# Kernel tuning notes

Measured on AMD Instinct MI355X. Metric: run time of the kernel, lower is better.

The kernel has to match this reference:

```python
import jax, jax.numpy as jnp
import numpy as np

EPS = 1e-06


def setup_inputs() -> dict:
    key = jax.random.key(0)
    ks = jax.random.split(key, 8)
    B, T, D = 4, 1024, 1024  # module requires T == D (diagonal einsum)
    s = 1.0 / np.sqrt(D)
    return {
        "x_seq": jax.random.normal(ks[0], (B, T, D), dtype=jnp.float32),
        "gamma": jnp.asarray(0.9, dtype=jnp.float32),
        "Wq": jax.random.normal(ks[1], (D, D), dtype=jnp.float32) * s,
        "bq": jax.random.normal(ks[2], (D,), dtype=jnp.float32) * 0.01,
        "Wk": jax.random.normal(ks[3], (D, D), dtype=jnp.float32) * s,
        "bk": jax.random.normal(ks[4], (D,), dtype=jnp.float32) * 0.01,
        "Wv": jax.random.normal(ks[5], (D, D), dtype=jnp.float32) * s,
        "bv": jax.random.normal(ks[6], (D,), dtype=jnp.float32) * 0.01,
    }


def reference(x_seq, gamma, Wq, bq, Wk, bk, Wv, bv):
    # Faithful math of SUPRAParallelFixedGamma.forward. Notes on fidelity:
    # - torch einsum 'ij,bjdj->bidj' takes the DIAGONAL of kv over (time, last
    #   v-dim), i.e. kv[b,j,d,j] = k[b,j,d] * v[b,j,j]; requires T == D.
    # - gamma_exponents = arange(T)[None,:] - arange(T)[:,None] -> E[i,j] = max(j-i, 0)
    #   (the clamp leaves PAST entries at gamma**0 == 1 and decays FUTURE ones).
    # - S = cumsum over dim 1 (the 'i'/time-output axis) then contracted with q;
    #   this factors exactly as C = cumsum(G, axis=0) applied as a (T,T) weight,
    #   avoiding the original's O(B*T*D*T) intermediate while computing the same math.
    B, T, D = x_seq.shape
    q = jax.nn.relu(x_seq @ Wq.T + bq)          # phi(W_q x)
    k = jax.nn.relu(x_seq @ Wk.T + bk)          # phi(W_k x)
    v = x_seq @ Wv.T + bv
    t = jnp.arange(T)
    E = jnp.maximum(t[None, :] - t[:, None], 0).astype(x_seq.dtype)  # (T,T)
    G = gamma ** E                               # gamma_powers[i,j] = gamma**max(j-i,0)
    C = jnp.cumsum(G, axis=0)                    # C[t,j] = sum_{t'<=t} G[t',j]
    vd = jnp.diagonal(v, axis1=1, axis2=2)       # (B,T): v[b,j,j]  (T==D)
    kv_diag = k * vd[:, :, None]                 # (B,T,D): kv[b,j,d,j]
    # num[b,t,j] = sum_d q[b,t,d] * C[t,j] * kv_diag[b,j,d]
    num = C[None, :, :] * jnp.einsum('btd,bjd->btj', q, kv_diag)
    # Z[b,t,d] = cumsum_t of (G @ k) = sum_j C[t,j] k[b,j,d]
    Z = jnp.einsum('tj,bjd->btd', C, k)
    denom = jnp.sum(q * Z, axis=-1, keepdims=True) + EPS
    return num / denom
```

## Files before the change

kernel.cpp:

```cpp
#include <hip/hip_runtime.h>

typedef __attribute__((ext_vector_type(8))) short bf16x8;
typedef __attribute__((ext_vector_type(4))) float f32x4;


__device__ __forceinline__ unsigned short f2bf(float f) {
    unsigned int u = __builtin_bit_cast(unsigned int, f);
    u += 0x7fffu + ((u >> 16) & 1u);
    return (unsigned short)(u >> 16);
}

__device__ __forceinline__ float bf2f(unsigned short s) {
    return __builtin_bit_cast(float, (unsigned int)s << 16);
}

__device__ __forceinline__ void g2lds16(const unsigned short* g, unsigned short* l) {
    __builtin_amdgcn_global_load_lds(
        (const __attribute__((address_space(1))) unsigned int*)g,
        (__attribute__((address_space(3))) unsigned int*)l, 16, 0, 0);
}


__global__ __launch_bounds__(256)
void prep_kernel(const float* __restrict__ x, const float* __restrict__ wq,
                 const float* __restrict__ wk, const float* __restrict__ Wv,
                 const float* __restrict__ bv, unsigned short* __restrict__ xb,
                 unsigned short* __restrict__ wqk, float* __restrict__ vd,
                 int n4x, int n4w, int npack) {
    if ((int)blockIdx.x < npack) {
        int i = blockIdx.x * 256 + threadIdx.x;
        const float* src; unsigned short* dst; int idx;
        if (i < n4x)            { src = x;  dst = xb;  idx = i; }
        else if (i < n4x + n4w) { src = wq; dst = wqk; idx = i - n4x; }
        else                    { src = wk; dst = wqk + (size_t)n4w * 4; idx = i - n4x - n4w; }
        float4 v = reinterpret_cast<const float4*>(src)[idx];
        union { unsigned short s[4]; uint2 u; } o;
        o.s[0] = f2bf(v.x); o.s[1] = f2bf(v.y); o.s[2] = f2bf(v.z); o.s[3] = f2bf(v.w);
        reinterpret_cast<uint2*>(dst)[idx] = o.u;
    } else {
        int w = (blockIdx.x - npack) * 4 + (threadIdx.x >> 6);
        int lane = threadIdx.x & 63;
        int b = w >> 10, j = w & 1023;
        const float4* xr = reinterpret_cast<const float4*>(x + (size_t)(b * 1024 + j) * 1024);
        const float4* wr = reinterpret_cast<const float4*>(Wv + (size_t)j * 1024);
        float s = 0.f;
        #pragma unroll
        for (int e = 0; e < 4; ++e) {
            float4 a = xr[lane + 64 * e], c = wr[lane + 64 * e];
            s += a.x * c.x + a.y * c.y + a.z * c.z + a.w * c.w;
        }
        #pragma unroll
        for (int off = 32; off; off >>= 1) s += __shfl_down(s, off, 64);
        if (lane == 0) vd[w] = s + bv[j];
    }
}


__global__ __launch_bounds__(256, 2)
void gemm_qk_kernel(const unsigned short* __restrict__ A, const unsigned short* __restrict__ Bm,
                    unsigned short* __restrict__ qb, unsigned short* __restrict__ kb,
                    const float* __restrict__ bq, const float* __restrict__ bk, int K) {
    __shared__ unsigned short lA[2][128 * 32];
    __shared__ unsigned short lB[2][128 * 32];

    const int tid = threadIdx.x;
    const int lane = tid & 63;
    const int wid = tid >> 6;
    const int wr = wid >> 1;
    const int wc = wid & 1;
    const int tileM = blockIdx.y * 128, tileN = blockIdx.x * 128;

    const int srow = tid >> 2;
    const int scolL = (tid & 3) * 8;
    const int scolG = ((tid & 3) ^ (srow & 3)) * 8;
    const int frow = lane & 15;
    const int fq = lane >> 4;
    const int gR = (fq ^ (frow & 3)) * 8;

    f32x4 acc[4][4];
    #pragma unroll
    for (int m = 0; m < 4; ++m)
        #pragma unroll
        for (int n = 0; n < 4; ++n)
            acc[m][n] = (f32x4){0.f, 0.f, 0.f, 0.f};

    auto stage = [&](int buf, int k0) {
        g2lds16(A + (size_t)(tileM + srow) * K + (k0 + scolG),      &lA[buf][srow * 32 + scolL]);
        g2lds16(A + (size_t)(tileM + 64 + srow) * K + (k0 + scolG), &lA[buf][(64 + srow) * 32 + scolL]);
        g2lds16(Bm + (size_t)(tileN + srow) * K + (k0 + scolG),     &lB[buf][srow * 32 + scolL]);
        g2lds16(Bm + (size_t)(tileN + 64 + srow) * K + (k0 + scolG),&lB[buf][(64 + srow) * 32 + scolL]);
    };

    stage(0, 0);
    __syncthreads();
    int cur = 0;
    for (int k0 = 0; k0 < K; k0 += 32) {
        if (k0 + 32 < K) stage(cur ^ 1, k0 + 32);

        bf16x8 af[4], bfr[4];
        #pragma unroll
        for (int m = 0; m < 4; ++m)
            af[m] = *reinterpret_cast<const bf16x8*>(
                &lA[cur][(wr * 64 + m * 16 + frow) * 32 + gR]);
        #pragma unroll
        for (int n = 0; n < 4; ++n)
            bfr[n] = *reinterpret_cast<const bf16x8*>(
                &lB[cur][(wc * 64 + n * 16 + frow) * 32 + gR]);

        #pragma unroll
        for (int m = 0; m < 4; ++m)
            #pragma unroll
            for (int n = 0; n < 4; ++n)
                acc[m][n] = __builtin_amdgcn_mfma_f32_16x16x32_bf16(af[m], bfr[n], acc[m][n], 0, 0, 0);

        __syncthreads();
        cur ^= 1;
    }

    const int orow = (lane >> 4) * 4;
    const int ocol = lane & 15;
    const bool isQ = tileN < 1024;
    unsigned short* Cq = isQ ? qb : kb;
    const float* bias = isQ ? bq : bk;
    const int cb = tileN - (isQ ? 0 : 1024);

    #pragma unroll
    for (int n = 0; n < 4; ++n) {
        int col = cb + wc * 64 + n * 16 + ocol;
        float bia = bias[col];
        #pragma unroll
        for (int m = 0; m < 4; ++m) {
            #pragma unroll
            for (int i = 0; i < 4; ++i) {
                int row = tileM + wr * 64 + m * 16 + orow + i;
                float v = acc[m][n][i] + bia;
                Cq[(size_t)row * 1024 + col] = f2bf(v > 0.f ? v : 0.f);
            }
        }
    }
}


__global__ __launch_bounds__(256, 3)
void gemm_attn_kernel(const unsigned short* __restrict__ A, const unsigned short* __restrict__ Bm,
                      unsigned short* __restrict__ nmb, const float* __restrict__ vd,
                      float* __restrict__ dpart, const float* __restrict__ gammap,
                      int K, int Mtot) {
    __shared__ unsigned short lA[2][64 * 32];
    __shared__ unsigned short lB[2][128 * 32];

    const int tid = threadIdx.x;
    const int lane = tid & 63;
    const int wid = tid >> 6;
    const int wr = wid >> 1, wc = wid & 1;
    const int tileM = blockIdx.y * 64, tileN = blockIdx.x * 128;

    const unsigned short* Ab = A + (size_t)blockIdx.z * 1024 * 1024;
    const unsigned short* Bb = Bm + (size_t)blockIdx.z * 1024 * 1024;

    const int r0 = tid >> 2;
    const int r1 = (tid + 256) >> 2;
    const int cc = (tid & 3) * 8;
    const int frow = lane & 15;
    const int fk = (lane >> 4) * 8;

    f32x4 acc[2][4];
    #pragma unroll
    for (int m = 0; m < 2; ++m)
        #pragma unroll
        for (int n = 0; n < 4; ++n)
            acc[m][n] = (f32x4){0.f, 0.f, 0.f, 0.f};

    auto stage = [&](int buf, int k0) {
        g2lds16(Ab + (size_t)(tileM + r0) * K + (k0 + cc), &lA[buf][tid * 8]);
        g2lds16(Bb + (size_t)(tileN + r0) * K + (k0 + cc), &lB[buf][tid * 8]);
        g2lds16(Bb + (size_t)(tileN + r1) * K + (k0 + cc), &lB[buf][2048 + tid * 8]);
    };

    stage(0, 0);
    __syncthreads();
    int cur = 0;
    for (int k0 = 0; k0 < K; k0 += 32) {
        if (k0 + 32 < K) stage(cur ^ 1, k0 + 32);

        bf16x8 af[2], bfr[4];
        #pragma unroll
        for (int m = 0; m < 2; ++m)
            af[m] = *reinterpret_cast<const bf16x8*>(&lA[cur][(wr * 32 + m * 16 + frow) * 32 + fk]);
        #pragma unroll
        for (int n = 0; n < 4; ++n)
            bfr[n] = *reinterpret_cast<const bf16x8*>(&lB[cur][(wc * 64 + n * 16 + frow) * 32 + fk]);

        #pragma unroll
        for (int m = 0; m < 2; ++m)
            #pragma unroll
            for (int n = 0; n < 4; ++n)
                acc[m][n] = __builtin_amdgcn_mfma_f32_16x16x32_bf16(af[m], bfr[n], acc[m][n], 0, 0, 0);

        __syncthreads();
        cur ^= 1;
    }

    const int orow = (lane >> 4) * 4;
    const int ocol = lane & 15;

    unsigned short* ob = nmb + (size_t)blockIdx.z * 1024 * 1024;
    const float* vdb = vd + blockIdx.z * 1024;
    const float g = gammap[0];
    const float l2g = log2f(g);
    const float inv1mg = 1.f / (1.f - g);
    const float c1 = g * inv1mg;

    int jcol[4]; float gj[4], vdv[4];
    #pragma unroll
    for (int n = 0; n < 4; ++n) {
        jcol[n] = tileN + wc * 64 + n * 16 + ocol;
        gj[n] = exp2f((float)jcol[n] * l2g);
        vdv[n] = vdb[jcol[n]];
    }

    #pragma unroll
    for (int m = 0; m < 2; ++m) {
        #pragma unroll
        for (int i = 0; i < 4; ++i) {
            int t = tileM + wr * 32 + m * 16 + orow + i;
            float gt = exp2f((float)t * l2g);
            float ctf = (1.f - g * gt) * inv1mg;
            float s = 0.f;
            #pragma unroll
            for (int n = 0; n < 4; ++n) {
                int j = jcol[n];
                float Cfut = exp2f((float)(j - t) * l2g) * ctf;
                float Cpast = (float)(t - j + 1) + c1 * (1.f - gj[n]);
                float Cw = (j <= t) ? Cpast : Cfut;
                float v = acc[m][n][i];
                s += Cw * v;
                ob[(size_t)t * 1024 + j] = f2bf(Cw * vdv[n] * v);
            }
            s += __shfl_xor(s, 1, 64);
            s += __shfl_xor(s, 2, 64);
            s += __shfl_xor(s, 4, 64);
            s += __shfl_xor(s, 8, 64);
            if ((lane & 15) == 0)
                dpart[(size_t)(blockIdx.x * 2 + wc) * Mtot + blockIdx.z * 1024 + t] = s;
        }
    }
}


__global__ __launch_bounds__(256)
void scale_kernel(const unsigned short* __restrict__ nmb, float* __restrict__ out,
                  const float* __restrict__ dpart, int Mtot) {
    int r = blockIdx.x;
    float s = 1e-6f;
    #pragma unroll
    for (int p = 0; p < 16; ++p) s += dpart[(size_t)p * Mtot + r];
    float inv = 1.f / s;
    const uint2* src = reinterpret_cast<const uint2*>(nmb + (size_t)r * 1024);
    float4* dst = reinterpret_cast<float4*>(out + (size_t)r * 1024);
    uint2 u = src[threadIdx.x];
    float4 v = { bf2f((unsigned short)(u.x & 0xffff)) * inv,
                 bf2f((unsigned short)(u.x >> 16))    * inv,
                 bf2f((unsigned short)(u.y & 0xffff)) * inv,
                 bf2f((unsigned short)(u.y >> 16))    * inv };
    dst[threadIdx.x] = v;
}


extern "C" void kernel_launch(void* const* d_in, const int* in_sizes, int n_in,
                              void* d_out, int out_size, void* d_ws, size_t ws_size,
                              hipStream_t stream) {
    const float* x     = (const float*)d_in[0];
    const float* gamma = (const float*)d_in[1];
    const float* Wq    = (const float*)d_in[2];
    const float* bq    = (const float*)d_in[3];
    const float* Wk    = (const float*)d_in[4];
    const float* bk    = (const float*)d_in[5];
    const float* Wv    = (const float*)d_in[6];
    const float* bv    = (const float*)d_in[7];
    float* out = (float*)d_out;

    const int D = 1024, T = 1024;
    const int B = in_sizes[0] / (T * D);
    const int M = B * T;

    char* ws = (char*)d_ws;
    size_t off = 0;
    unsigned short* xb  = (unsigned short*)(ws + off); off += (size_t)M * D * 2;
    unsigned short* wqk = (unsigned short*)(ws + off); off += (size_t)2 * D * D * 2;
    unsigned short* qb  = (unsigned short*)(ws + off); off += (size_t)M * D * 2;
    unsigned short* kb  = (unsigned short*)(ws + off); off += (size_t)M * D * 2;
    float* vd    = (float*)(ws + off); off += (size_t)M * 4;
    float* dpart = (float*)(ws + off); off += (size_t)16 * M * 4;
    unsigned short* nmb = xb;

    const int n4x = M * D / 4, n4w = D * D / 4;
    const int npack = (n4x + 2 * n4w) / 256;

    prep_kernel<<<dim3(npack + M / 4), 256, 0, stream>>>(
        x, Wq, Wk, Wv, bv, xb, wqk, vd, n4x, n4w, npack);

    gemm_qk_kernel<<<dim3(2048 / 128, M / 128), 256, 0, stream>>>(
        xb, wqk, qb, kb, bq, bk, D);

    gemm_attn_kernel<<<dim3(T / 128, T / 64, B), 256, 0, stream>>>(
        qb, kb, nmb, vd, dpart, gamma, D, M);

    scale_kernel<<<dim3(M), 256, 0, stream>>>(nmb, out, dpart, M);
}
```

Measured before the change: 75.13 us.

## Enlarge QK GEMM tiles to 256x256 with 4-slot async LDS pipeline

The Q/K projection GEMM moves from 128x128 tiles with 256 threads and double buffering to 256x256 tiles with 512 threads, a 4-slot LDS ring that prefetches two stages ahead, and explicit vmcnt waits with a single barrier per k-step. The MFMA loop is raised in priority via s_setprio, and A fragments are loaded per m-row to limit register pressure. The aim is more reuse per LDS load and better overlap of global-to-LDS copies with MFMA. The trade-offs are that the XOR swizzle is dropped, which may cause LDS bank conflicts, LDS use grows to 128 KB, and the grid shrinks to 128 blocks, which may underfill the GPU.

```diff
diff --git a/kernel.cpp b/kernel.cpp
--- a/kernel.cpp
+++ b/kernel.cpp
@@ -56,65 +56,71 @@
 }
 
 
-__global__ __launch_bounds__(256, 2)
+__global__ __launch_bounds__(512, 2)
 void gemm_qk_kernel(const unsigned short* __restrict__ A, const unsigned short* __restrict__ Bm,
                     unsigned short* __restrict__ qb, unsigned short* __restrict__ kb,
                     const float* __restrict__ bq, const float* __restrict__ bk, int K) {
-    __shared__ unsigned short lA[2][128 * 32];
-    __shared__ unsigned short lB[2][128 * 32];
+    __shared__ unsigned short lA[4][256 * 32];
+    __shared__ unsigned short lB[4][256 * 32];
 
     const int tid = threadIdx.x;
     const int lane = tid & 63;
     const int wid = tid >> 6;
-    const int wr = wid >> 1;
-    const int wc = wid & 1;
-    const int tileM = blockIdx.y * 128, tileN = blockIdx.x * 128;
-
-    const int srow = tid >> 2;
-    const int scolL = (tid & 3) * 8;
-    const int scolG = ((tid & 3) ^ (srow & 3)) * 8;
+    const int wm = wid >> 2;
+    const int wn = wid & 3;
+    const int tileM = blockIdx.y * 256, tileN = blockIdx.x * 256;
+
     const int frow = lane & 15;
-    const int fq = lane >> 4;
-    const int gR = (fq ^ (frow & 3)) * 8;
-
-    f32x4 acc[4][4];
-    #pragma unroll
-    for (int m = 0; m < 4; ++m)
+    const int fq8 = (lane >> 4) * 8;
+
+    const int sr0 = wid * 16 + (lane >> 2);
+    const int sc = (lane & 3) * 8;
+
+    f32x4 acc[8][4];
+    #pragma unroll
+    for (int m = 0; m < 8; ++m)
         #pragma unroll
         for (int n = 0; n < 4; ++n)
             acc[m][n] = (f32x4){0.f, 0.f, 0.f, 0.f};
 
-    auto stage = [&](int buf, int k0) {
-        g2lds16(A + (size_t)(tileM + srow) * K + (k0 + scolG),      &lA[buf][srow * 32 + scolL]);
-        g2lds16(A + (size_t)(tileM + 64 + srow) * K + (k0 + scolG), &lA[buf][(64 + srow) * 32 + scolL]);
-        g2lds16(Bm + (size_t)(tileN + srow) * K + (k0 + scolG),     &lB[buf][srow * 32 + scolL]);
-        g2lds16(Bm + (size_t)(tileN + 64 + srow) * K + (k0 + scolG),&lB[buf][(64 + srow) * 32 + scolL]);
+    auto stage = [&](int slot, int k0) {
+        #pragma unroll
+        for (int j = 0; j < 2; ++j) {
+            int r = sr0 + j * 128;
+            g2lds16(A + (size_t)(tileM + r) * K + (k0 + sc), &lA[slot][r * 32 + sc]);
+            g2lds16(Bm + (size_t)(tileN + r) * K + (k0 + sc), &lB[slot][r * 32 + sc]);
+        }
     };
 
+    const int nS = K >> 5;
     stage(0, 0);
-    __syncthreads();
-    int cur = 0;
-    for (int k0 = 0; k0 < K; k0 += 32) {
-        if (k0 + 32 < K) stage(cur ^ 1, k0 + 32);
-
-        bf16x8 af[4], bfr[4];
-        #pragma unroll
-        for (int m = 0; m < 4; ++m)
-            af[m] = *reinterpret_cast<const bf16x8*>(
-                &lA[cur][(wr * 64 + m * 16 + frow) * 32 + gR]);
+    stage(1, 32);
+
+    for (int s = 0; s < nS; ++s) {
+        const int slot = s & 3;
+        if (s + 1 < nS) asm volatile("s_waitcnt vmcnt(4)" ::: "memory");
+        else            asm volatile("s_waitcnt vmcnt(0)" ::: "memory");
+        __builtin_amdgcn_s_barrier();
+        asm volatile("" ::: "memory");
+
+        if (s + 2 < nS) stage((s + 2) & 3, (s + 2) << 5);
+
+        bf16x8 bfr[4];
         #pragma unroll
         for (int n = 0; n < 4; ++n)
             bfr[n] = *reinterpret_cast<const bf16x8*>(
-                &lB[cur][(wc * 64 + n * 16 + frow) * 32 + gR]);
-
-        #pragma unroll
-        for (int m = 0; m < 4; ++m)
+                &lB[slot][(wn * 64 + n * 16 + frow) * 32 + fq8]);
+
+        __builtin_amdgcn_s_setprio(1);
+        #pragma unroll
+        for (int m = 0; m < 8; ++m) {
+            bf16x8 af = *reinterpret_cast<const bf16x8*>(
+                &lA[slot][(wm * 128 + m * 16 + frow) * 32 + fq8]);
             #pragma unroll
             for (int n = 0; n < 4; ++n)
-                acc[m][n] = __builtin_amdgcn_mfma_f32_16x16x32_bf16(af[m], bfr[n], acc[m][n], 0, 0, 0);
-
-        __syncthreads();
-        cur ^= 1;
+                acc[m][n] = __builtin_amdgcn_mfma_f32_16x16x32_bf16(af, bfr[n], acc[m][n], 0, 0, 0);
+        }
+        __builtin_amdgcn_s_setprio(0);
     }
 
     const int orow = (lane >> 4) * 4;
@@ -126,13 +132,13 @@
 
     #pragma unroll
     for (int n = 0; n < 4; ++n) {
-        int col = cb + wc * 64 + n * 16 + ocol;
+        int col = cb + wn * 64 + n * 16 + ocol;
         float bia = bias[col];
         #pragma unroll
-        for (int m = 0; m < 4; ++m) {
+        for (int m = 0; m < 8; ++m) {
             #pragma unroll
             for (int i = 0; i < 4; ++i) {
-                int row = tileM + wr * 64 + m * 16 + orow + i;
+                int row = tileM + wm * 128 + m * 16 + orow + i;
                 float v = acc[m][n][i] + bia;
                 Cq[(size_t)row * 1024 + col] = f2bf(v > 0.f ? v : 0.f);
             }
@@ -300,7 +306,7 @@
     prep_kernel<<<dim3(npack + M / 4), 256, 0, stream>>>(
         x, Wq, Wk, Wv, bv, xb, wqk, vd, n4x, n4w, npack);
 
-    gemm_qk_kernel<<<dim3(2048 / 128, M / 128), 256, 0, stream>>>(
+    gemm_qk_kernel<<<dim3(2048 / 256, M / 256), 512, 0, stream>>>(
         xb, wqk, qb, kb, bq, bk, D);
 
     gemm_attn_kernel<<<dim3(T / 128, T / 64, B), 256, 0, stream>>>(
```

Measured after the change: 92.68 us. 23.4% more time.
